# Optimization experiments

Measured on AMD Instinct MI355X. Metric: run time of the kernel, lower is better.

## Reference

```python
import jax, jax.numpy as jnp
import numpy as np

S, B, I, H = 2048, 4096, 2, 6  # seq, batch, input_size, hidden_size


def setup_inputs() -> dict:
    key = jax.random.key(0)
    ks = jax.random.split(key, 11)
    init = lambda k, sh: jax.random.normal(k, sh, dtype=jnp.float32) * 0.1
    return {
        "x": jax.random.normal(ks[0], (S, B, I), dtype=jnp.float32),
        # layer-0 LSTM params (PyTorch gate order: i, f, g, o)
        "Wih0": init(ks[1], (4 * H, I)),
        "Whh0": init(ks[2], (4 * H, H)),
        "bih0": init(ks[3], (4 * H,)),
        "bhh0": init(ks[4], (4 * H,)),
        # layer-1 LSTM params
        "Wih1": init(ks[5], (4 * H, H)),
        "Whh1": init(ks[6], (4 * H, H)),
        "bih1": init(ks[7], (4 * H,)),
        "bhh1": init(ks[8], (4 * H,)),
        # final Linear(6, 1)
        "W2": init(ks[9], (1, H)),
        "b2": init(ks[10], (1,)),
    }


def _lstm_layer(x, Wih, Whh, bih, bhh):
    # x: (S, B, in_dim) -> hidden outputs (S, B, H)
    Bn = x.shape[1]
    Hn = Whh.shape[1]
    b = bih + bhh
    # precompute input projections for all timesteps at once (memory-bound GEMM)
    xg = jnp.einsum("sbi,gi->sbg", x, Wih) + b  # (S, B, 4H)

    def step(carry, xt_g):
        h, c = carry
        g = xt_g + h @ Whh.T  # (B, 4H)
        i, f, gg, o = jnp.split(g, 4, axis=-1)
        i = jax.nn.sigmoid(i)
        f = jax.nn.sigmoid(f)
        gg = jnp.tanh(gg)
        o = jax.nn.sigmoid(o)
        c = f * c + i * gg
        h = o * jnp.tanh(c)
        return (h, c), h

    h0 = jnp.zeros((Bn, Hn), dtype=x.dtype)
    c0 = jnp.zeros((Bn, Hn), dtype=x.dtype)
    _, hs = jax.lax.scan(step, (h0, c0), xg)
    return hs  # (S, B, H)


def reference(x, Wih0, Whh0, bih0, bhh0, Wih1, Whh1, bih1, bhh1, W2, b2):
    h1 = _lstm_layer(x, Wih0, Whh0, bih0, bhh0)   # (S, B, H)
    h2 = _lstm_layer(h1, Wih1, Whh1, bih1, bhh1)  # (S, B, H); dropout disabled (eval)
    flat = h2.reshape(-1, H)                       # (S*B, H)
    out = flat @ W2.T + b2                         # (S*B, 1) — original discards final view
    return out
```

## Files before the change

### kernel.cpp

```cpp
#include <hip/hip_runtime.h>

#define SEQ   2048
#define BATCH 4096
#define HID   6
#define BLK   256

typedef float v2f __attribute__((ext_vector_type(2)));
typedef unsigned u2 __attribute__((ext_vector_type(2)));

__device__ __forceinline__ float fexp2(float a) {
#if __has_builtin(__builtin_amdgcn_exp2f)
  return __builtin_amdgcn_exp2f(a);
#else
  float r; asm("v_exp_f32 %0, %1" : "=v"(r) : "v"(a)); return r;
#endif
}
__device__ __forceinline__ float frcp(float a) {
#if __has_builtin(__builtin_amdgcn_rcpf)
  return __builtin_amdgcn_rcpf(a);
#else
  float r; asm("v_rcp_f32 %0, %1" : "=v"(r) : "v"(a)); return r;
#endif
}

template <int OFF>
__device__ __forceinline__ float swzf(float v) {
  int r = __builtin_amdgcn_ds_swizzle(__builtin_bit_cast(int, v), OFF);
  return __builtin_bit_cast(float, r);
}
#define BC0 0x18
#define BC1 0x38
#define BC2 0x58
#define BC3 0x78
#define BC4 0x98
#define BC5 0xB8

__device__ __forceinline__ float xhalf(float v, bool hi) {
#if __has_builtin(__builtin_amdgcn_permlane32_swap)
  u2 r = __builtin_amdgcn_permlane32_swap(__builtin_bit_cast(unsigned, v),
                                          __builtin_bit_cast(unsigned, v), false, false);
  return __builtin_bit_cast(float, hi ? r.x : r.y);
#else
  unsigned d = __builtin_bit_cast(unsigned, v), s = d;
  asm volatile("v_permlane32_swap_b32 %0, %1" : "+v"(d), "+v"(s));
  return __builtin_bit_cast(float, hi ? d : s);
#endif
}

__global__ __launch_bounds__(BLK, 1) void lstm2_kernel(
    const float* __restrict__ x,
    const float* __restrict__ Wih0, const float* __restrict__ Whh0,
    const float* __restrict__ bih0, const float* __restrict__ bhh0,
    const float* __restrict__ Wih1, const float* __restrict__ Whh1,
    const float* __restrict__ bih1, const float* __restrict__ bhh1,
    const float* __restrict__ W2,   const float* __restrict__ b2,
    float* __restrict__ out)
{
  __shared__ float obuf[64][16];

  const int tid = threadIdx.x;
  const int wib = tid >> 6;
  const int l6  = tid & 63;
  const bool hi = l6 >= 32;
  const int j   = l6 & 31;
  const int el  = j >> 3;
  const int u   = j & 7;
  const int uu  = (u < HID) ? u : (HID - 1);
  const int b   = blockIdx.x * 16 + wib * 4 + el;

  v2f WA[4][3], WB[4][3];
  float BS[4];
#pragma unroll
  for (int q = 0; q < 4; ++q) {
    const int rq = q * HID + uu;
    const float Kq = (q == 2) ? -2.8853900817779268f : -1.4426950408889634f;
    if (!hi) {
      WA[q][0] = v2f{Kq * Wih0[rq * 2 + 0], Kq * Wih0[rq * 2 + 1]};
      WA[q][1] = v2f{0.f, 0.f};
      WA[q][2] = v2f{0.f, 0.f};
#pragma unroll
      for (int k = 0; k < 3; ++k)
        WB[q][k] = v2f{Kq * Whh0[rq * HID + 2 * k], Kq * Whh0[rq * HID + 2 * k + 1]};
      BS[q] = Kq * (bih0[rq] + bhh0[rq]);
    } else {
#pragma unroll
      for (int k = 0; k < 3; ++k) {
        WA[q][k] = v2f{Kq * Wih1[rq * HID + 2 * k], Kq * Wih1[rq * HID + 2 * k + 1]};
        WB[q][k] = v2f{Kq * Whh1[rq * HID + 2 * k], Kq * Whh1[rq * HID + 2 * k + 1]};
      }
      BS[q] = Kq * (bih1[rq] + bhh1[rq]);
    }
  }
  const v2f w2p0 = v2f{W2[0], W2[1]}, w2p1 = v2f{W2[2], W2[3]}, w2p2 = v2f{W2[4], W2[5]};
  const float bout = b2[0];
  const float KT = 2.8853900817779268f;

  float h = 0.f, c = 0.f;

  auto gath = [&](float hv, v2f (&g)[3]) {
    g[0] = v2f{swzf<BC0>(hv), swzf<BC1>(hv)};
    g[1] = v2f{swzf<BC2>(hv), swzf<BC3>(hv)};
    g[2] = v2f{swzf<BC4>(hv), swzf<BC5>(hv)};
  };

  auto step = [&](v2f xc, float& ov) {
    v2f g2[3]; gath(h, g2);
    float hs = xhalf(h, hi);
    v2f g1[3]; gath(hs, g1);
    v2f v10 = hi ? g1[0] : xc;

    float a[4];
#pragma unroll
    for (int q = 0; q < 4; ++q) {
      v2f acc = v2f{BS[q], 0.f};
      acc = __builtin_elementwise_fma(WA[q][0], v10,   acc);
      acc = __builtin_elementwise_fma(WA[q][1], g1[1], acc);
      acc = __builtin_elementwise_fma(WA[q][2], g1[2], acc);
      acc = __builtin_elementwise_fma(WB[q][0], g2[0], acc);
      acc = __builtin_elementwise_fma(WB[q][1], g2[1], acc);
      acc = __builtin_elementwise_fma(WB[q][2], g2[2], acc);
      a[q] = acc.x + acc.y;
    }
    v2f ao = __builtin_elementwise_fma(w2p0, g2[0],
             __builtin_elementwise_fma(w2p1, g2[1],
             __builtin_elementwise_fma(w2p2, g2[2], v2f{bout, 0.f})));
    ov = ao.x + ao.y;

    float i_ = frcp(1.f + fexp2(a[0]));
    float f_ = frcp(1.f + fexp2(a[1]));
    float g_ = fmaf(2.f, frcp(1.f + fexp2(a[2])), -1.f);
    float o_ = frcp(1.f + fexp2(a[3]));
    c = fmaf(f_, c, i_ * g_);
    float th = fmaf(-2.f, frcp(1.f + fexp2(c * KT)), 1.f);
    h = o_ * th;
  };

  auto flush = [&](int rbase) {
    const int r = tid >> 2, jj = (tid & 3) * 4;
    float4 vv = *(const float4*)&obuf[r][jj];
    *(float4*)&out[(size_t)(rbase + r) * BATCH + blockIdx.x * 16 + jj] = vv;
  };

  const v2f* x2 = (const v2f*)x;
  v2f xc  = x2[(size_t)0 * BATCH + b];
  v2f xn1 = x2[(size_t)1 * BATCH + b];
  v2f xn2 = x2[(size_t)2 * BATCH + b];
  v2f xn3 = x2[(size_t)3 * BATCH + b];

  {
    float ov;
    step(xc, ov);
    if (hi) { h = 0.f; c = 0.f; }
    v2f xf = x2[(size_t)4 * BATCH + b];
    xc = xn1; xn1 = xn2; xn2 = xn3; xn3 = xf;
  }

#pragma unroll 1
  for (int t = 1; t < SEQ; ++t) {
    int tf = t + 4; tf = (tf < SEQ) ? tf : (SEQ - 1);
    v2f xf = x2[(size_t)tf * BATCH + b];

    float ov;
    step(xc, ov);

    if (t >= 2) {
      const int r = t - 2;
      if (hi && u == 0) obuf[r & 63][wib * 4 + el] = ov;
      if ((r & 63) == 63) {
        __syncthreads();
        flush(r - 63);
        __syncthreads();
      }
    }
    xc = xn1; xn1 = xn2; xn2 = xn3; xn3 = xf;
  }

  {
    float ov;
    step(xc, ov);
    if (hi && u == 0) obuf[62][wib * 4 + el] = ov;
    v2f g2[3]; gath(h, g2);
    v2f ao = __builtin_elementwise_fma(w2p0, g2[0],
             __builtin_elementwise_fma(w2p1, g2[1],
             __builtin_elementwise_fma(w2p2, g2[2], v2f{bout, 0.f})));
    if (hi && u == 0) obuf[63][wib * 4 + el] = ao.x + ao.y;
    __syncthreads();
    flush(SEQ - 64);
  }
}

extern "C" void kernel_launch(void* const* d_in, const int* in_sizes, int n_in,
                              void* d_out, int out_size, void* d_ws, size_t ws_size,
                              hipStream_t stream) {
  const float* x    = (const float*)d_in[0];
  const float* Wih0 = (const float*)d_in[1];
  const float* Whh0 = (const float*)d_in[2];
  const float* bih0 = (const float*)d_in[3];
  const float* bhh0 = (const float*)d_in[4];
  const float* Wih1 = (const float*)d_in[5];
  const float* Whh1 = (const float*)d_in[6];
  const float* bih1 = (const float*)d_in[7];
  const float* bhh1 = (const float*)d_in[8];
  const float* W2   = (const float*)d_in[9];
  const float* b2   = (const float*)d_in[10];
  float* out = (float*)d_out;

  dim3 grid(BATCH / 16);
  dim3 block(BLK);
  hipLaunchKernelGGL(lstm2_kernel, grid, block, 0, stream,
                     x, Wih0, Whh0, bih0, bhh0, Wih1, Whh1, bih1, bhh1, W2, b2, out);
}
```

Before: 621.0 us.

## Interleave two batch elements per lane and stage x chunks in LDS

```diff
diff --git a/kernel.cpp b/kernel.cpp
--- a/kernel.cpp
+++ b/kernel.cpp
@@ -56,7 +56,8 @@
     const float* __restrict__ W2,   const float* __restrict__ b2,
     float* __restrict__ out)
 {
-  __shared__ float obuf[64][16];
+  __shared__ float obuf[64][32];
+  __shared__ float xbuf[2][64][64];
 
   const int tid = threadIdx.x;
   const int wib = tid >> 6;
@@ -66,7 +67,8 @@
   const int el  = j >> 3;
   const int u   = j & 7;
   const int uu  = (u < HID) ? u : (HID - 1);
-  const int b   = blockIdx.x * 16 + wib * 4 + el;
+  const int eA  = wib * 8 + el;
+  const int eB  = eA + 4;
 
   v2f WA[4][3], WB[4][3];
   float BS[4];
@@ -95,7 +97,7 @@
   const float bout = b2[0];
   const float KT = 2.8853900817779268f;
 
-  float h = 0.f, c = 0.f;
+  float hA = 0.f, cA = 0.f, hB = 0.f, cB = 0.f;
 
   auto gath = [&](float hv, v2f (&g)[3]) {
     g[0] = v2f{swzf<BC0>(hv), swzf<BC1>(hv)};
@@ -103,87 +105,155 @@
     g[2] = v2f{swzf<BC4>(hv), swzf<BC5>(hv)};
   };
 
-  auto step = [&](v2f xc, float& ov) {
-    v2f g2[3]; gath(h, g2);
-    float hs = xhalf(h, hi);
-    v2f g1[3]; gath(hs, g1);
-    v2f v10 = hi ? g1[0] : xc;
-
-    float a[4];
+  auto step2 = [&](v2f xA, v2f xB, float& ovA, float& ovB) {
+    v2f GA[3], GB[3];
+    gath(hA, GA);
+    gath(hB, GB);
+    v2f HA[3], HB[3];
+#pragma unroll
+    for (int k = 0; k < 3; ++k) {
+      HA[k] = v2f{xhalf(GA[k].x, hi), xhalf(GA[k].y, hi)};
+      HB[k] = v2f{xhalf(GB[k].x, hi), xhalf(GB[k].y, hi)};
+    }
+    v2f vA = hi ? HA[0] : xA;
+    v2f vB = hi ? HB[0] : xB;
+
+    float aA[4], aB[4];
 #pragma unroll
     for (int q = 0; q < 4; ++q) {
-      v2f acc = v2f{BS[q], 0.f};
-      acc = __builtin_elementwise_fma(WA[q][0], v10,   acc);
-      acc = __builtin_elementwise_fma(WA[q][1], g1[1], acc);
-      acc = __builtin_elementwise_fma(WA[q][2], g1[2], acc);
-      acc = __builtin_elementwise_fma(WB[q][0], g2[0], acc);
-      acc = __builtin_elementwise_fma(WB[q][1], g2[1], acc);
-      acc = __builtin_elementwise_fma(WB[q][2], g2[2], acc);
-      a[q] = acc.x + acc.y;
-    }
-    v2f ao = __builtin_elementwise_fma(w2p0, g2[0],
-             __builtin_elementwise_fma(w2p1, g2[1],
-             __builtin_elementwise_fma(w2p2, g2[2], v2f{bout, 0.f})));
-    ov = ao.x + ao.y;
-
-    float i_ = frcp(1.f + fexp2(a[0]));
-    float f_ = frcp(1.f + fexp2(a[1]));
-    float g_ = fmaf(2.f, frcp(1.f + fexp2(a[2])), -1.f);
-    float o_ = frcp(1.f + fexp2(a[3]));
-    c = fmaf(f_, c, i_ * g_);
-    float th = fmaf(-2.f, frcp(1.f + fexp2(c * KT)), 1.f);
-    h = o_ * th;
+      v2f p = __builtin_elementwise_fma(WA[q][0], vA, v2f{BS[q], 0.f});
+      p = __builtin_elementwise_fma(WA[q][1], HA[1], p);
+      p = __builtin_elementwise_fma(WA[q][2], HA[2], p);
+      v2f r = WB[q][0] * GA[0];
+      r = __builtin_elementwise_fma(WB[q][1], GA[1], r);
+      r = __builtin_elementwise_fma(WB[q][2], GA[2], r);
+      v2f s = p + r;
+      aA[q] = s.x + s.y;
+    }
+#pragma unroll
+    for (int q = 0; q < 4; ++q) {
+      v2f p = __builtin_elementwise_fma(WA[q][0], vB, v2f{BS[q], 0.f});
+      p = __builtin_elementwise_fma(WA[q][1], HB[1], p);
+      p = __builtin_elementwise_fma(WA[q][2], HB[2], p);
+      v2f r = WB[q][0] * GB[0];
+      r = __builtin_elementwise_fma(WB[q][1], GB[1], r);
+      r = __builtin_elementwise_fma(WB[q][2], GB[2], r);
+      v2f s = p + r;
+      aB[q] = s.x + s.y;
+    }
+
+    v2f aoA = __builtin_elementwise_fma(w2p0, GA[0],
+              __builtin_elementwise_fma(w2p1, GA[1],
+              __builtin_elementwise_fma(w2p2, GA[2], v2f{bout, 0.f})));
+    ovA = aoA.x + aoA.y;
+    v2f aoB = __builtin_elementwise_fma(w2p0, GB[0],
+              __builtin_elementwise_fma(w2p1, GB[1],
+              __builtin_elementwise_fma(w2p2, GB[2], v2f{bout, 0.f})));
+    ovB = aoB.x + aoB.y;
+
+    float iA = frcp(1.f + fexp2(aA[0]));
+    float fA = frcp(1.f + fexp2(aA[1]));
+    float gA = fmaf(2.f, frcp(1.f + fexp2(aA[2])), -1.f);
+    float oA = frcp(1.f + fexp2(aA[3]));
+    float iB = frcp(1.f + fexp2(aB[0]));
+    float fB = frcp(1.f + fexp2(aB[1]));
+    float gB = fmaf(2.f, frcp(1.f + fexp2(aB[2])), -1.f);
+    float oB = frcp(1.f + fexp2(aB[3]));
+    cA = fmaf(fA, cA, iA * gA);
+    cB = fmaf(fB, cB, iB * gB);
+    float tA = fmaf(-2.f, frcp(1.f + fexp2(cA * KT)), 1.f);
+    float tB = fmaf(-2.f, frcp(1.f + fexp2(cB * KT)), 1.f);
+    hA = oA * tA;
+    hB = oB * tB;
   };
 
   auto flush = [&](int rbase) {
-    const int r = tid >> 2, jj = (tid & 3) * 4;
-    float4 vv = *(const float4*)&obuf[r][jj];
-    *(float4*)&out[(size_t)(rbase + r) * BATCH + blockIdx.x * 16 + jj] = vv;
+#pragma unroll
+    for (int k = 0; k < 2; ++k) {
+      const int f = tid * 2 + k;
+      const int row = f >> 3, off = (f & 7) * 4;
+      float4 vv = *(const float4*)&obuf[row][off];
+      *(float4*)&out[(size_t)(rbase + row) * BATCH + blockIdx.x * 32 + off] = vv;
+    }
   };
 
-  const v2f* x2 = (const v2f*)x;
-  v2f xc  = x2[(size_t)0 * BATCH + b];
-  v2f xn1 = x2[(size_t)1 * BATCH + b];
-  v2f xn2 = x2[(size_t)2 * BATCH + b];
-  v2f xn3 = x2[(size_t)3 * BATCH + b];
-
   {
-    float ov;
-    step(xc, ov);
-    if (hi) { h = 0.f; c = 0.f; }
-    v2f xf = x2[(size_t)4 * BATCH + b];
-    xc = xn1; xn1 = xn2; xn2 = xn3; xn3 = xf;
+    const int row = tid >> 2, cb = (tid & 3) * 16;
+    const float* s0 = x + (size_t)row * (BATCH * 2) + blockIdx.x * 64 + cb;
+    const float* s1 = s0 + (size_t)64 * (BATCH * 2);
+    float4 a0 = *(const float4*)(s0 + 0),  a1 = *(const float4*)(s0 + 4);
+    float4 a2 = *(const float4*)(s0 + 8),  a3 = *(const float4*)(s0 + 12);
+    float4 b0 = *(const float4*)(s1 + 0),  b1 = *(const float4*)(s1 + 4);
+    float4 b2v = *(const float4*)(s1 + 8), b3 = *(const float4*)(s1 + 12);
+    *(float4*)&xbuf[0][row][cb + 0]  = a0;  *(float4*)&xbuf[0][row][cb + 4]  = a1;
+    *(float4*)&xbuf[0][row][cb + 8]  = a2;  *(float4*)&xbuf[0][row][cb + 12] = a3;
+    *(float4*)&xbuf[1][row][cb + 0]  = b0;  *(float4*)&xbuf[1][row][cb + 4]  = b1;
+    *(float4*)&xbuf[1][row][cb + 8]  = b2v; *(float4*)&xbuf[1][row][cb + 12] = b3;
+    __syncthreads();
+  }
+
+  v2f xrA = *(const v2f*)&xbuf[0][0][eA * 2];
+  v2f xrB = *(const v2f*)&xbuf[0][0][eB * 2];
+
+  {
+    float ovA, ovB;
+    step2(xrA, xrB, ovA, ovB);
+    if (hi) { hA = 0.f; cA = 0.f; hB = 0.f; cB = 0.f; }
+    xrA = *(const v2f*)&xbuf[0][1][eA * 2];
+    xrB = *(const v2f*)&xbuf[0][1][eB * 2];
   }
 
 #pragma unroll 1
   for (int t = 1; t < SEQ; ++t) {
-    int tf = t + 4; tf = (tf < SEQ) ? tf : (SEQ - 1);
-    v2f xf = x2[(size_t)tf * BATCH + b];
-
-    float ov;
-    step(xc, ov);
+    const int tn = (t + 1 < SEQ) ? t + 1 : SEQ - 1;
+    v2f xnA = *(const v2f*)&xbuf[(tn >> 6) & 1][tn & 63][eA * 2];
+    v2f xnB = *(const v2f*)&xbuf[(tn >> 6) & 1][tn & 63][eB * 2];
+
+    float ovA, ovB;
+    step2(xrA, xrB, ovA, ovB);
 
     if (t >= 2) {
       const int r = t - 2;
-      if (hi && u == 0) obuf[r & 63][wib * 4 + el] = ov;
+      if (hi && u == 0) { obuf[r & 63][eA] = ovA; obuf[r & 63][eB] = ovB; }
       if ((r & 63) == 63) {
+        const int ck = (t >> 6) + 1;
+        const bool doR = (ck * 64 < SEQ);
+        const int row = tid >> 2, cb = (tid & 3) * 16;
+        float4 r0, r1, r2, r3;
+        if (doR) {
+          const float* src = x + ((size_t)(ck * 64) + row) * (BATCH * 2)
+                               + blockIdx.x * 64 + cb;
+          r0 = *(const float4*)(src + 0);  r1 = *(const float4*)(src + 4);
+          r2 = *(const float4*)(src + 8);  r3 = *(const float4*)(src + 12);
+        }
         __syncthreads();
         flush(r - 63);
+        if (doR) {
+          *(float4*)&xbuf[ck & 1][row][cb + 0]  = r0;
+          *(float4*)&xbuf[ck & 1][row][cb + 4]  = r1;
+          *(float4*)&xbuf[ck & 1][row][cb + 8]  = r2;
+          *(float4*)&xbuf[ck & 1][row][cb + 12] = r3;
+        }
         __syncthreads();
       }
     }
-    xc = xn1; xn1 = xn2; xn2 = xn3; xn3 = xf;
+    xrA = xnA; xrB = xnB;
   }
 
   {
-    float ov;
-    step(xc, ov);
-    if (hi && u == 0) obuf[62][wib * 4 + el] = ov;
-    v2f g2[3]; gath(h, g2);
-    v2f ao = __builtin_elementwise_fma(w2p0, g2[0],
-             __builtin_elementwise_fma(w2p1, g2[1],
-             __builtin_elementwise_fma(w2p2, g2[2], v2f{bout, 0.f})));
-    if (hi && u == 0) obuf[63][wib * 4 + el] = ao.x + ao.y;
+    float ovA, ovB;
+    step2(xrA, xrB, ovA, ovB);
+    if (hi && u == 0) { obuf[62][eA] = ovA; obuf[62][eB] = ovB; }
+    v2f GA[3], GB[3];
+    gath(hA, GA);
+    gath(hB, GB);
+    v2f aoA = __builtin_elementwise_fma(w2p0, GA[0],
+              __builtin_elementwise_fma(w2p1, GA[1],
+              __builtin_elementwise_fma(w2p2, GA[2], v2f{bout, 0.f})));
+    v2f aoB = __builtin_elementwise_fma(w2p0, GB[0],
+              __builtin_elementwise_fma(w2p1, GB[1],
+              __builtin_elementwise_fma(w2p2, GB[2], v2f{bout, 0.f})));
+    if (hi && u == 0) { obuf[63][eA] = aoA.x + aoA.y; obuf[63][eB] = aoB.x + aoB.y; }
     __syncthreads();
     flush(SEQ - 64);
   }
@@ -205,7 +275,7 @@
   const float* b2   = (const float*)d_in[10];
   float* out = (float*)d_out;
 
-  dim3 grid(BATCH / 16);
+  dim3 grid(BATCH / 32);
   dim3 block(BLK);
   hipLaunchKernelGGL(lstm2_kernel, grid, block, 0, stream,
                      x, Wih0, Whh0, bih0, bhh0, Wih1, Whh1, bih1, bhh1, W2, b2, out);
```

Measured after the change: 1.090 ms. +75.6%, slower.

## Pack two batch elements per lane and gather hidden state with DPP

Applied to the files above, without the earlier changes.

```diff
diff --git a/kernel.cpp b/kernel.cpp
--- a/kernel.cpp
+++ b/kernel.cpp
@@ -3,7 +3,7 @@
 #define SEQ   2048
 #define BATCH 4096
 #define HID   6
-#define BLK   256
+#define BLK   128
 
 typedef float v2f __attribute__((ext_vector_type(2)));
 typedef unsigned u2 __attribute__((ext_vector_type(2)));
@@ -22,18 +22,15 @@
   float r; asm("v_rcp_f32 %0, %1" : "=v"(r) : "v"(a)); return r;
 #endif
 }
-
-template <int OFF>
-__device__ __forceinline__ float swzf(float v) {
-  int r = __builtin_amdgcn_ds_swizzle(__builtin_bit_cast(int, v), OFF);
+__device__ __forceinline__ v2f exp2v(v2f a) { return v2f{fexp2(a.x), fexp2(a.y)}; }
+__device__ __forceinline__ v2f rcpv(v2f a)  { return v2f{frcp(a.x), frcp(a.y)}; }
+__device__ __forceinline__ v2f sp(float w)  { return v2f{w, w}; }
+
+template <int CTRL>
+__device__ __forceinline__ float dppf(float v) {
+  int r = __builtin_amdgcn_update_dpp(0, __builtin_bit_cast(int, v), CTRL, 0xF, 0xF, true);
   return __builtin_bit_cast(float, r);
 }
-#define BC0 0x18
-#define BC1 0x38
-#define BC2 0x58
-#define BC3 0x78
-#define BC4 0x98
-#define BC5 0xB8
 
 __device__ __forceinline__ float xhalf(float v, bool hi) {
 #if __has_builtin(__builtin_amdgcn_permlane32_swap)
@@ -62,128 +59,144 @@
   const int wib = tid >> 6;
   const int l6  = tid & 63;
   const bool hi = l6 >= 32;
-  const int j   = l6 & 31;
-  const int el  = j >> 3;
-  const int u   = j & 7;
+  const int pp  = (l6 >> 3) & 3;
+  const int u   = l6 & 7;
   const int uu  = (u < HID) ? u : (HID - 1);
-  const int b   = blockIdx.x * 16 + wib * 4 + el;
-
-  v2f WA[4][3], WB[4][3];
-  float BS[4];
+  const int gp  = wib * 4 + pp;
+
+  float WR[4][8], WI[4][8], w2s[8], BS[4];
 #pragma unroll
   for (int q = 0; q < 4; ++q) {
     const int rq = q * HID + uu;
     const float Kq = (q == 2) ? -2.8853900817779268f : -1.4426950408889634f;
+#pragma unroll
+    for (int k = 0; k < 8; ++k) {
+      const int kk = u ^ k;
+      const bool ok = (kk < HID);
+      WR[q][k] = ok ? Kq * (hi ? Whh1[rq * HID + kk] : Whh0[rq * HID + kk]) : 0.f;
+      WI[q][k] = (hi && ok) ? Kq * Wih1[rq * HID + kk] : 0.f;
+    }
     if (!hi) {
-      WA[q][0] = v2f{Kq * Wih0[rq * 2 + 0], Kq * Wih0[rq * 2 + 1]};
-      WA[q][1] = v2f{0.f, 0.f};
-      WA[q][2] = v2f{0.f, 0.f};
-#pragma unroll
-      for (int k = 0; k < 3; ++k)
-        WB[q][k] = v2f{Kq * Whh0[rq * HID + 2 * k], Kq * Whh0[rq * HID + 2 * k + 1]};
-      BS[q] = Kq * (bih0[rq] + bhh0[rq]);
-    } else {
-#pragma unroll
-      for (int k = 0; k < 3; ++k) {
-        WA[q][k] = v2f{Kq * Wih1[rq * HID + 2 * k], Kq * Wih1[rq * HID + 2 * k + 1]};
-        WB[q][k] = v2f{Kq * Whh1[rq * HID + 2 * k], Kq * Whh1[rq * HID + 2 * k + 1]};
-      }
-      BS[q] = Kq * (bih1[rq] + bhh1[rq]);
-    }
-  }
-  const v2f w2p0 = v2f{W2[0], W2[1]}, w2p1 = v2f{W2[2], W2[3]}, w2p2 = v2f{W2[4], W2[5]};
+      WI[q][0] = Kq * Wih0[rq * 2 + 0];
+      WI[q][1] = Kq * Wih0[rq * 2 + 1];
+    }
+    BS[q] = Kq * ((hi ? bih1[rq] : bih0[rq]) + (hi ? bhh1[rq] : bhh0[rq]));
+  }
+#pragma unroll
+  for (int k = 0; k < 8; ++k) {
+    const int kk = u ^ k;
+    w2s[k] = (kk < HID) ? W2[kk] : 0.f;
+  }
   const float bout = b2[0];
-  const float KT = 2.8853900817779268f;
-
-  float h = 0.f, c = 0.f;
-
-  auto gath = [&](float hv, v2f (&g)[3]) {
-    g[0] = v2f{swzf<BC0>(hv), swzf<BC1>(hv)};
-    g[1] = v2f{swzf<BC2>(hv), swzf<BC3>(hv)};
-    g[2] = v2f{swzf<BC4>(hv), swzf<BC5>(hv)};
+  const v2f ONE = v2f{1.f, 1.f};
+  const v2f KTv = v2f{2.8853900817779268f, 2.8853900817779268f};
+
+  v2f h = v2f{0.f, 0.f}, c = v2f{0.f, 0.f};
+
+  auto gathc = [&](v2f hv, v2f (&g)[8]) {
+    float hx = hv.x, hy = hv.y;
+    float tx1 = dppf<0xB1>(hx),  ty1 = dppf<0xB1>(hy);
+    float tx2 = dppf<0x4E>(hx),  ty2 = dppf<0x4E>(hy);
+    float tx3 = dppf<0x4E>(tx1), ty3 = dppf<0x4E>(ty1);
+    float mx  = dppf<0x141>(hx), my  = dppf<0x141>(hy);
+    float mx1 = dppf<0xB1>(mx),  my1 = dppf<0xB1>(my);
+    float mx2 = dppf<0x4E>(mx),  my2 = dppf<0x4E>(my);
+    float mx3 = dppf<0x4E>(mx1), my3 = dppf<0x4E>(my1);
+    g[0] = v2f{hx,  hy};  g[1] = v2f{tx1, ty1};
+    g[2] = v2f{tx2, ty2}; g[3] = v2f{tx3, ty3};
+    g[4] = v2f{mx3, my3}; g[5] = v2f{mx2, my2};
+    g[6] = v2f{mx1, my1}; g[7] = v2f{mx,  my};
   };
 
-  auto step = [&](v2f xc, float& ov) {
-    v2f g2[3]; gath(h, g2);
-    float hs = xhalf(h, hi);
-    v2f g1[3]; gath(hs, g1);
-    v2f v10 = hi ? g1[0] : xc;
-
-    float a[4];
+  auto step = [&](v2f xp0, v2f xp1, v2f& ov) {
+    v2f g2[8]; gathc(h, g2);
+    v2f g1[8];
+#pragma unroll
+    for (int k = 0; k < 8; ++k)
+      g1[k] = v2f{xhalf(g2[k].x, hi), xhalf(g2[k].y, hi)};
+    v2f in0 = hi ? g1[0] : xp0;
+    v2f in1 = hi ? g1[1] : xp1;
+
+    v2f a[4];
 #pragma unroll
     for (int q = 0; q < 4; ++q) {
-      v2f acc = v2f{BS[q], 0.f};
-      acc = __builtin_elementwise_fma(WA[q][0], v10,   acc);
-      acc = __builtin_elementwise_fma(WA[q][1], g1[1], acc);
-      acc = __builtin_elementwise_fma(WA[q][2], g1[2], acc);
-      acc = __builtin_elementwise_fma(WB[q][0], g2[0], acc);
-      acc = __builtin_elementwise_fma(WB[q][1], g2[1], acc);
-      acc = __builtin_elementwise_fma(WB[q][2], g2[2], acc);
-      a[q] = acc.x + acc.y;
-    }
-    v2f ao = __builtin_elementwise_fma(w2p0, g2[0],
-             __builtin_elementwise_fma(w2p1, g2[1],
-             __builtin_elementwise_fma(w2p2, g2[2], v2f{bout, 0.f})));
-    ov = ao.x + ao.y;
-
-    float i_ = frcp(1.f + fexp2(a[0]));
-    float f_ = frcp(1.f + fexp2(a[1]));
-    float g_ = fmaf(2.f, frcp(1.f + fexp2(a[2])), -1.f);
-    float o_ = frcp(1.f + fexp2(a[3]));
-    c = fmaf(f_, c, i_ * g_);
-    float th = fmaf(-2.f, frcp(1.f + fexp2(c * KT)), 1.f);
+      v2f acc = sp(BS[q]);
+      acc = __builtin_elementwise_fma(sp(WI[q][0]), in0, acc);
+      acc = __builtin_elementwise_fma(sp(WI[q][1]), in1, acc);
+#pragma unroll
+      for (int k = 2; k < 8; ++k)
+        acc = __builtin_elementwise_fma(sp(WI[q][k]), g1[k], acc);
+#pragma unroll
+      for (int k = 0; k < 8; ++k)
+        acc = __builtin_elementwise_fma(sp(WR[q][k]), g2[k], acc);
+      a[q] = acc;
+    }
+    v2f ao = sp(bout);
+#pragma unroll
+    for (int k = 0; k < 8; ++k)
+      ao = __builtin_elementwise_fma(sp(w2s[k]), g2[k], ao);
+    ov = ao;
+
+    v2f i_ = rcpv(ONE + exp2v(a[0]));
+    v2f f_ = rcpv(ONE + exp2v(a[1]));
+    v2f g_ = __builtin_elementwise_fma(sp(2.f), rcpv(ONE + exp2v(a[2])), sp(-1.f));
+    v2f o_ = rcpv(ONE + exp2v(a[3]));
+    c = __builtin_elementwise_fma(f_, c, i_ * g_);
+    v2f th = __builtin_elementwise_fma(sp(-2.f), rcpv(ONE + exp2v(c * KTv)), ONE);
     h = o_ * th;
   };
 
   auto flush = [&](int rbase) {
-    const int r = tid >> 2, jj = (tid & 3) * 4;
-    float4 vv = *(const float4*)&obuf[r][jj];
-    *(float4*)&out[(size_t)(rbase + r) * BATCH + blockIdx.x * 16 + jj] = vv;
+    const int row = tid >> 1, half = (tid & 1) * 8;
+    float4 v0 = *(const float4*)&obuf[row][half];
+    float4 v1 = *(const float4*)&obuf[row][half + 4];
+    float* dst = &out[(size_t)(rbase + row) * BATCH + blockIdx.x * 16 + half];
+    *(float4*)dst = v0;
+    *(float4*)(dst + 4) = v1;
   };
 
-  const v2f* x2 = (const v2f*)x;
-  v2f xc  = x2[(size_t)0 * BATCH + b];
-  v2f xn1 = x2[(size_t)1 * BATCH + b];
-  v2f xn2 = x2[(size_t)2 * BATCH + b];
-  v2f xn3 = x2[(size_t)3 * BATCH + b];
+  const float4* x4 = (const float4*)x;
+  const size_t xidx = (size_t)blockIdx.x * 8 + gp;
+  float4 xc4 = x4[xidx], xn4 = x4[(size_t)1 * 2048 + xidx];
 
   {
-    float ov;
-    step(xc, ov);
-    if (hi) { h = 0.f; c = 0.f; }
-    v2f xf = x2[(size_t)4 * BATCH + b];
-    xc = xn1; xn1 = xn2; xn2 = xn3; xn3 = xf;
+    v2f ov;
+    step(v2f{xc4.x, xc4.z}, v2f{xc4.y, xc4.w}, ov);
+    if (hi) { h = v2f{0.f, 0.f}; c = v2f{0.f, 0.f}; }
+    xc4 = xn4;
+    xn4 = x4[(size_t)2 * 2048 + xidx];
   }
 
 #pragma unroll 1
   for (int t = 1; t < SEQ; ++t) {
-    int tf = t + 4; tf = (tf < SEQ) ? tf : (SEQ - 1);
-    v2f xf = x2[(size_t)tf * BATCH + b];
-
-    float ov;
-    step(xc, ov);
+    const int tn = (t + 2 < SEQ) ? t + 2 : SEQ - 1;
+    float4 xf4 = x4[(size_t)tn * 2048 + xidx];
+
+    v2f ov;
+    step(v2f{xc4.x, xc4.z}, v2f{xc4.y, xc4.w}, ov);
 
     if (t >= 2) {
       const int r = t - 2;
-      if (hi && u == 0) obuf[r & 63][wib * 4 + el] = ov;
+      if (hi && u == 0) *(v2f*)&obuf[r & 63][gp * 2] = ov;
       if ((r & 63) == 63) {
         __syncthreads();
         flush(r - 63);
         __syncthreads();
       }
     }
-    xc = xn1; xn1 = xn2; xn2 = xn3; xn3 = xf;
+    xc4 = xn4; xn4 = xf4;
   }
 
   {
-    float ov;
-    step(xc, ov);
-    if (hi && u == 0) obuf[62][wib * 4 + el] = ov;
-    v2f g2[3]; gath(h, g2);
-    v2f ao = __builtin_elementwise_fma(w2p0, g2[0],
-             __builtin_elementwise_fma(w2p1, g2[1],
-             __builtin_elementwise_fma(w2p2, g2[2], v2f{bout, 0.f})));
-    if (hi && u == 0) obuf[63][wib * 4 + el] = ao.x + ao.y;
+    v2f ov;
+    step(v2f{xc4.x, xc4.z}, v2f{xc4.y, xc4.w}, ov);
+    if (hi && u == 0) *(v2f*)&obuf[62][gp * 2] = ov;
+    v2f g2[8]; gathc(h, g2);
+    v2f ao = sp(bout);
+#pragma unroll
+    for (int k = 0; k < 8; ++k)
+      ao = __builtin_elementwise_fma(sp(w2s[k]), g2[k], ao);
+    if (hi && u == 0) *(v2f*)&obuf[63][gp * 2] = ao;
     __syncthreads();
     flush(SEQ - 64);
   }
```

Result: slower. 1.134 ms (+82.6%).
